# Kernel optimization log

Measured on AMD Instinct MI355X. Metric: run time of the kernel, lower is better.

## Reference

```python
import jax, jax.numpy as jnp
import numpy as np


def setup_inputs() -> dict:
    key = jax.random.key(0)
    k1, k2, k3 = jax.random.split(key, 3)
    B, H, W = 4, 1080, 1920
    Sh, Sw, Sl = 16, 16, 8
    pixels = jax.random.uniform(k1, (B, H, W, 3), dtype=jnp.float32)
    coords = jax.random.uniform(k2, (B, H, W, 2), dtype=jnp.float32)
    # identity affine grid + small perturbation (learned parameter)
    identity = jnp.zeros((Sh, Sw, Sl, 12), dtype=jnp.float32)
    identity = identity.at[..., 0].set(1.0).at[..., 5].set(1.0).at[..., 10].set(1.0)
    grid = identity + 0.1 * jax.random.normal(k3, (Sh, Sw, Sl, 12), dtype=jnp.float32)
    return {"pixels": pixels, "coords": coords, "grid": grid}


def _bilateral_apply(pixels, coords, grid):
    orig_shape = pixels.shape[:-1]
    p = pixels.reshape(-1, 3)        # (N, 3)
    c = coords.reshape(-1, 2)        # (N, 2)
    Sh, Sw, Sl = grid.shape[0], grid.shape[1], grid.shape[2]

    # guide = luminance
    guide = 0.2126 * p[:, 0] + 0.7152 * p[:, 1] + 0.0722 * p[:, 2]

    gx = jnp.clip(c[:, 0] * (Sw - 1), 0.0, Sw - 1.001)
    gy = jnp.clip(c[:, 1] * (Sh - 1), 0.0, Sh - 1.001)
    gz = jnp.clip(jnp.clip(guide, 0.0, 1.0) * (Sl - 1), 0.0, Sl - 1.001)

    y0 = jnp.floor(gy).astype(jnp.int32)
    x0 = jnp.floor(gx).astype(jnp.int32)
    z0 = jnp.floor(gz).astype(jnp.int32)
    y1 = jnp.minimum(y0 + 1, Sh - 1)
    x1 = jnp.minimum(x0 + 1, Sw - 1)
    z1 = jnp.minimum(z0 + 1, Sl - 1)

    fy = (gy - y0.astype(gy.dtype))[:, None]
    fx = (gx - x0.astype(gx.dtype))[:, None]
    fz = (gz - z0.astype(gz.dtype))[:, None]

    c000 = grid[y0, x0, z0]
    c001 = grid[y0, x0, z1]
    c010 = grid[y0, x1, z0]
    c011 = grid[y0, x1, z1]
    c100 = grid[y1, x0, z0]
    c101 = grid[y1, x0, z1]
    c110 = grid[y1, x1, z0]
    c111 = grid[y1, x1, z1]

    c00 = c000 + (c001 - c000) * fz
    c01 = c010 + (c011 - c010) * fz
    c10 = c100 + (c101 - c100) * fz
    c11 = c110 + (c111 - c110) * fz
    c0 = c00 + (c01 - c00) * fx
    c1 = c10 + (c11 - c10) * fx
    coeffs = c0 + (c1 - c0) * fy      # (N, 12)

    A = coeffs.reshape(-1, 3, 4)
    # affine: A[:, :, :3] @ rgb + A[:, :, 3]  (equivalent to cat with ones)
    out = jnp.einsum('nij,nj->ni', A[:, :, :3], p) + A[:, :, 3]
    return out.reshape(*orig_shape, 3)


def reference(pixels, coords, grid):
    return _bilateral_apply(pixels, coords, grid)
```

## Files before the change

### kernel.cpp

```cpp
#include <hip/hip_runtime.h>


typedef _Float16 h2 __attribute__((ext_vector_type(2)));
typedef _Float16 h4 __attribute__((ext_vector_type(4)));

#define BLOCK 512
#define ZS 12
#define XS 100
#define YS 1604
#define NLDS (16 * YS)

__global__ __launch_bounds__(BLOCK) void bilateral_apply(
    const float* __restrict__ pixels,
    const float* __restrict__ coords,
    const float* __restrict__ grid,
    float* __restrict__ out,
    int n4)
{
    __shared__ _Float16 gl[NLDS];

    {
        for (int cell = threadIdx.x; cell < 2048; cell += BLOCK) {
            int y = cell >> 7;
            int x = (cell >> 3) & 15;
            int z = cell & 7;
            const float4* src = (const float4*)(grid + (long long)cell * 12);
            float4 v0 = src[0], v1 = src[1], v2 = src[2];
            h4* d = (h4*)(gl + y * YS + x * XS + z * ZS);
            d[0] = h4{(_Float16)v0.x, (_Float16)v0.y, (_Float16)v0.z, (_Float16)v0.w};
            d[1] = h4{(_Float16)v1.x, (_Float16)v1.y, (_Float16)v1.z, (_Float16)v1.w};
            d[2] = h4{(_Float16)v2.x, (_Float16)v2.y, (_Float16)v2.z, (_Float16)v2.w};
        }
    }
    __syncthreads();

    const int stride = gridDim.x * BLOCK;
    for (int t = blockIdx.x * BLOCK + threadIdx.x; t < n4; t += stride) {
        long long base = (long long)t * 4;

        const float* pp = pixels + base * 3;
        const float* cp = coords + base * 2;
        float4 pa = *(const float4*)(pp + 0);
        float4 pb = *(const float4*)(pp + 4);
        float4 pc = *(const float4*)(pp + 8);
        float4 ca = *(const float4*)(cp + 0);
        float4 cb = *(const float4*)(cp + 4);

        float R[4]  = {pa.x, pa.w, pb.z, pc.y};
        float G[4]  = {pa.y, pb.x, pb.w, pc.z};
        float Bc[4] = {pa.z, pb.y, pc.x, pc.w};
        float CX[4] = {ca.x, ca.z, cb.x, cb.z};
        float CY[4] = {ca.y, ca.w, cb.y, cb.w};

        float O[12];

        #pragma unroll
        for (int k = 0; k < 4; ++k) {
            float r = R[k], g = G[k], b = Bc[k];
            float guide = 0.2126f * r + 0.7152f * g + 0.0722f * b;

            float gx = fminf(fmaxf(CX[k] * 15.0f, 0.0f), 14.999f);
            float gy = fminf(fmaxf(CY[k] * 15.0f, 0.0f), 14.999f);
            float gz = fminf(fminf(fmaxf(guide, 0.0f), 1.0f) * 7.0f, 6.999f);

            int x0 = (int)gx, y0 = (int)gy, z0 = (int)gz;
            float fx = gx - (float)x0;
            float fy = gy - (float)y0;
            float fz = gz - (float)z0;

            int cbase = y0 * YS + x0 * XS + z0 * ZS;
            const int coff[4] = {0, XS, YS, YS + XS};
            float wz0 = 1.0f - fz, wz1 = fz;
            float cw[4] = {(1.0f - fy) * (1.0f - fx), (1.0f - fy) * fx,
                           fy * (1.0f - fx),           fy * fx};

            h4 acc0 = (h4)(_Float16)0.0f;
            h4 acc1 = (h4)(_Float16)0.0f;
            h4 acc2 = (h4)(_Float16)0.0f;

            #pragma unroll
            for (int c = 0; c < 4; ++c) {
                const h4* q = (const h4*)(gl + cbase + coff[c]);
                h4 a0 = q[0], a1 = q[1], a2 = q[2];
                h4 b0 = q[3], b1 = q[4], b2 = q[5];
                _Float16 u0 = (_Float16)(cw[c] * wz0);
                _Float16 u1 = (_Float16)(cw[c] * wz1);
                h4 u0v = {u0, u0, u0, u0};
                h4 u1v = {u1, u1, u1, u1};
                acc0 = a0 * u0v + (b0 * u1v + acc0);
                acc1 = a1 * u0v + (b1 * u1v + acc1);
                acc2 = a2 * u0v + (b2 * u1v + acc2);
            }

            O[3 * k + 0] = fmaf((float)acc0.x, r, fmaf((float)acc0.y, g,
                           fmaf((float)acc0.z, b, (float)acc0.w)));
            O[3 * k + 1] = fmaf((float)acc1.x, r, fmaf((float)acc1.y, g,
                           fmaf((float)acc1.z, b, (float)acc1.w)));
            O[3 * k + 2] = fmaf((float)acc2.x, r, fmaf((float)acc2.y, g,
                           fmaf((float)acc2.z, b, (float)acc2.w)));
        }

        float* op = out + base * 3;
        *(float4*)(op + 0) = make_float4(O[0], O[1], O[2],  O[3]);
        *(float4*)(op + 4) = make_float4(O[4], O[5], O[6],  O[7]);
        *(float4*)(op + 8) = make_float4(O[8], O[9], O[10], O[11]);
    }
}

extern "C" void kernel_launch(void* const* d_in, const int* in_sizes, int n_in,
                              void* d_out, int out_size, void* d_ws, size_t ws_size,
                              hipStream_t stream) {
    const float* pixels = (const float*)d_in[0];
    const float* coords = (const float*)d_in[1];
    const float* grid   = (const float*)d_in[2];
    float* out = (float*)d_out;

    int npix = in_sizes[0] / 3;
    int n4   = npix / 4;
    int nblk = 768;
    bilateral_apply<<<nblk, BLOCK, 0, stream>>>(pixels, coords, grid, out, n4);
}
```

Baseline: 232.1 us.

## Split LDS grid into two 16-byte-aligned arrays for wide h8 loads

Splits the fp16 grid in shared memory into two arrays. One holds coefficients 0-7 per z cell, so a z0/z1 pair is two consecutive 16-byte loads. The other holds coefficients 8-11 with z and z+1 interleaved, so both fit in one 16-byte load. This cuts LDS load instructions per corner from six 8-byte reads to three 16-byte reads. It also raises the block size to 1024 with launch bounds hinting 8 blocks and lowers the block count to 512, which changes occupancy and register pressure and may cause spills or bank conflicts.

Result: slower. 269.3 us (+16.0%).

```diff
diff --git a/kernel.cpp b/kernel.cpp
--- a/kernel.cpp
+++ b/kernel.cpp
@@ -1,36 +1,41 @@
 #include <hip/hip_runtime.h>
 
 
-typedef _Float16 h2 __attribute__((ext_vector_type(2)));
 typedef _Float16 h4 __attribute__((ext_vector_type(4)));
+typedef _Float16 h8 __attribute__((ext_vector_type(8)));
 
-#define BLOCK 512
-#define ZS 12
-#define XS 100
-#define YS 1604
-#define NLDS (16 * YS)
+#define BLOCK 1024
 
-__global__ __launch_bounds__(BLOCK) void bilateral_apply(
+#define XSA 72
+#define YSA 1152
+#define NA  18432
+#define XSB 56
+#define YSB 896
+#define NB  14336
+
+__global__ __launch_bounds__(BLOCK, 8) void bilateral_apply(
     const float* __restrict__ pixels,
     const float* __restrict__ coords,
     const float* __restrict__ grid,
     float* __restrict__ out,
     int n4)
 {
-    __shared__ _Float16 gl[NLDS];
+    __shared__ alignas(16) _Float16 gA[NA];
+    __shared__ alignas(16) _Float16 gB[NB];
 
-    {
-        for (int cell = threadIdx.x; cell < 2048; cell += BLOCK) {
-            int y = cell >> 7;
-            int x = (cell >> 3) & 15;
-            int z = cell & 7;
-            const float4* src = (const float4*)(grid + (long long)cell * 12);
-            float4 v0 = src[0], v1 = src[1], v2 = src[2];
-            h4* d = (h4*)(gl + y * YS + x * XS + z * ZS);
-            d[0] = h4{(_Float16)v0.x, (_Float16)v0.y, (_Float16)v0.z, (_Float16)v0.w};
-            d[1] = h4{(_Float16)v1.x, (_Float16)v1.y, (_Float16)v1.z, (_Float16)v1.w};
-            d[2] = h4{(_Float16)v2.x, (_Float16)v2.y, (_Float16)v2.z, (_Float16)v2.w};
-        }
+    for (int cell = threadIdx.x; cell < 2048; cell += BLOCK) {
+        int y = cell >> 7;
+        int x = (cell >> 3) & 15;
+        int z = cell & 7;
+        const float4* src = (const float4*)(grid + (long long)cell * 12);
+        float4 v0 = src[0], v1 = src[1], v2 = src[2];
+        h8 a = { (_Float16)v0.x, (_Float16)v0.y, (_Float16)v0.z, (_Float16)v0.w,
+                 (_Float16)v1.x, (_Float16)v1.y, (_Float16)v1.z, (_Float16)v1.w };
+        *(h8*)(gA + y * YSA + x * XSA + z * 8) = a;
+        h4 b = { (_Float16)v2.x, (_Float16)v2.y, (_Float16)v2.z, (_Float16)v2.w };
+        _Float16* bb = gB + y * YSB + x * XSB;
+        if (z <= 6) *(h4*)(bb + z * 8) = b;
+        if (z >= 1) *(h4*)(bb + (z - 1) * 8 + 4) = b;
     }
     __syncthreads();
 
@@ -68,36 +73,44 @@
             float fy = gy - (float)y0;
             float fz = gz - (float)z0;
 
-            int cbase = y0 * YS + x0 * XS + z0 * ZS;
-            const int coff[4] = {0, XS, YS, YS + XS};
+            int abase = y0 * YSA + x0 * XSA + z0 * 8;
+            int bbase = y0 * YSB + x0 * XSB + z0 * 8;
+            const int aoff[4] = {0, XSA, YSA, YSA + XSA};
+            const int boff[4] = {0, XSB, YSB, YSB + XSB};
             float wz0 = 1.0f - fz, wz1 = fz;
             float cw[4] = {(1.0f - fy) * (1.0f - fx), (1.0f - fy) * fx,
                            fy * (1.0f - fx),           fy * fx};
 
-            h4 acc0 = (h4)(_Float16)0.0f;
-            h4 acc1 = (h4)(_Float16)0.0f;
-            h4 acc2 = (h4)(_Float16)0.0f;
+            h8 accA = (h8)(_Float16)0.0f;
+            h4 accB = (h4)(_Float16)0.0f;
 
             #pragma unroll
             for (int c = 0; c < 4; ++c) {
-                const h4* q = (const h4*)(gl + cbase + coff[c]);
-                h4 a0 = q[0], a1 = q[1], a2 = q[2];
-                h4 b0 = q[3], b1 = q[4], b2 = q[5];
+                const h8* qa = (const h8*)(gA + abase + aoff[c]);
+                h8 alo = qa[0];
+                h8 ahi = qa[1];
+                h8 qb  = *(const h8*)(gB + bbase + boff[c]);
                 _Float16 u0 = (_Float16)(cw[c] * wz0);
                 _Float16 u1 = (_Float16)(cw[c] * wz1);
-                h4 u0v = {u0, u0, u0, u0};
-                h4 u1v = {u1, u1, u1, u1};
-                acc0 = a0 * u0v + (b0 * u1v + acc0);
-                acc1 = a1 * u0v + (b1 * u1v + acc1);
-                acc2 = a2 * u0v + (b2 * u1v + acc2);
+                h8 u0v8 = {u0, u0, u0, u0, u0, u0, u0, u0};
+                h8 u1v8 = {u1, u1, u1, u1, u1, u1, u1, u1};
+                accA = alo * u0v8 + (ahi * u1v8 + accA);
+                h4 blo = __builtin_shufflevector(qb, qb, 0, 1, 2, 3);
+                h4 bhi = __builtin_shufflevector(qb, qb, 4, 5, 6, 7);
+                h4 u0v4 = {u0, u0, u0, u0};
+                h4 u1v4 = {u1, u1, u1, u1};
+                accB = blo * u0v4 + (bhi * u1v4 + accB);
             }
+
+            h4 acc0 = __builtin_shufflevector(accA, accA, 0, 1, 2, 3);
+            h4 acc1 = __builtin_shufflevector(accA, accA, 4, 5, 6, 7);
 
             O[3 * k + 0] = fmaf((float)acc0.x, r, fmaf((float)acc0.y, g,
                            fmaf((float)acc0.z, b, (float)acc0.w)));
             O[3 * k + 1] = fmaf((float)acc1.x, r, fmaf((float)acc1.y, g,
                            fmaf((float)acc1.z, b, (float)acc1.w)));
-            O[3 * k + 2] = fmaf((float)acc2.x, r, fmaf((float)acc2.y, g,
-                           fmaf((float)acc2.z, b, (float)acc2.w)));
+            O[3 * k + 2] = fmaf((float)accB.x, r, fmaf((float)accB.y, g,
+                           fmaf((float)accB.z, b, (float)accB.w)));
         }
 
         float* op = out + base * 3;
@@ -117,6 +130,6 @@
 
     int npix = in_sizes[0] / 3;
     int n4   = npix / 4;
-    int nblk = 768;
+    int nblk = 512;
     bilateral_apply<<<nblk, BLOCK, 0, stream>>>(pixels, coords, grid, out, n4);
 }
```
